# Kernel optimization log

Hardware: AMD Instinct MI355X
Metric: run time of the kernel (lower is better)

## Reference

```python
import jax, jax.numpy as jnp
import numpy as np

N_NODES = 100000


def sage_conv(x, src, dst, w_self, w_nei, b):
    # mean aggregation over incoming edges (src -> dst)
    agg = jax.ops.segment_sum(x[src], dst, num_segments=N_NODES)          # [N, d]
    deg = jax.ops.segment_sum(jnp.ones((src.shape[0], 1), x.dtype), dst,
                              num_segments=N_NODES)                        # [N, 1]
    mean = agg / jnp.maximum(deg, 1.0)
    return x @ w_self + mean @ w_nei + b


def setup_inputs() -> dict:
    key = jax.random.key(0)
    ks = jax.random.split(key, 12)
    d_in, d_hid, d_out = 64, 64, 64
    E = 1600000
    s = lambda d: 1.0 / np.sqrt(d)
    return {
        "x": jax.random.normal(ks[0], (N_NODES, d_in), jnp.float32),
        "edge_index": jax.random.randint(ks[1], (2, E), 0, N_NODES, jnp.int64),
        "w_self1": jax.random.normal(ks[2], (d_in, d_hid), jnp.float32) * s(d_in),
        "w_nei1": jax.random.normal(ks[3], (d_in, d_hid), jnp.float32) * s(d_in),
        "b1": jnp.zeros((d_hid,), jnp.float32),
        "w_self2": jax.random.normal(ks[4], (d_hid, d_hid), jnp.float32) * s(d_hid),
        "w_nei2": jax.random.normal(ks[5], (d_hid, d_hid), jnp.float32) * s(d_hid),
        "b2": jnp.zeros((d_hid,), jnp.float32),
        "w_self3": jax.random.normal(ks[6], (d_hid, d_out), jnp.float32) * s(d_hid),
        "w_nei3": jax.random.normal(ks[7], (d_hid, d_out), jnp.float32) * s(d_hid),
        "b3": jnp.zeros((d_out,), jnp.float32),
    }


def reference(x, edge_index, w_self1, w_nei1, b1, w_self2, w_nei2, b2,
              w_self3, w_nei3, b3):
    src, dst = edge_index[0], edge_index[1]
    h = jax.nn.relu(sage_conv(x, src, dst, w_self1, w_nei1, b1))
    h = jax.nn.relu(sage_conv(h, src, dst, w_self2, w_nei2, b2))
    h = sage_conv(h, src, dst, w_self3, w_nei3, b3)
    return h
```

## Files before the change

kernel.cpp:

```cpp
#include <hip/hip_runtime.h>
#include <hip/hip_bf16.h>

#define PB   512
#define BN   64
#define CAP  1344

typedef short bf16x8 __attribute__((ext_vector_type(8)));
typedef float f32x4  __attribute__((ext_vector_type(4)));

__device__ __forceinline__ unsigned short f2bf(float f) {
    unsigned u = __float_as_uint(f);
    u += 0x7FFFu + ((u >> 16) & 1u);
    return (unsigned short)(u >> 16);
}

__global__ __launch_bounds__(256) void build_and_prep(
        const int* __restrict__ src, const int* __restrict__ dst,
        int* __restrict__ gcount, int* __restrict__ pairs, int E, int NB,
        const float* __restrict__ x,
        unsigned short* __restrict__ xlo, unsigned short* __restrict__ xhi, int n8,
        const float* __restrict__ Ws1, const float* __restrict__ Wn1,
        const float* __restrict__ Ws2, const float* __restrict__ Wn2,
        const float* __restrict__ Ws3, const float* __restrict__ Wn3,
        unsigned short* __restrict__ bw) {
    const int tid = threadIdx.x;
    if (blockIdx.x < PB) {
        __shared__ int h[1664];
        for (int i = tid; i < NB; i += 256) h[i] = 0;
        __syncthreads();
        const int per = (E + PB - 1) / PB;
        const int s = blockIdx.x * per;
        const int e = min(E, s + per);
        for (int i = s + tid; i < e; i += 256) atomicAdd(&h[dst[i] >> 6], 1);
        __syncthreads();
        for (int b = tid; b < NB; b += 256) {
            const int c = h[b];
            h[b] = (c > 0) ? atomicAdd(&gcount[b], c) : 0;
        }
        __syncthreads();
        for (int i = s + tid; i < e; i += 256) {
            const int d = dst[i];
            const int b = d >> 6;
            const int slot = atomicAdd(&h[b], 1);
            if (slot < CAP)
                pairs[(size_t)b * CAP + slot] = src[i] | ((d & 63) << 20);
        }
    } else if (blockIdx.x < PB + 96) {
        const int i = (blockIdx.x - PB) * 256 + tid;
        const int w = i >> 13;
        const int r = i & 8191;
        const float* Ws = (w == 0) ? Ws1 : (w == 1) ? Ws2 : Ws3;
        const float* Wn = (w == 0) ? Wn1 : (w == 1) ? Wn2 : Wn3;
        const int j = r & 7;
        const int L = (r >> 3) & 63;
        const int t = (r >> 9) & 3;
        const int s = r >> 11;
        const int k = s * 32 + ((L >> 4) << 3) + j;
        const int n = t * 16 + (L & 15);
        const float v = (k < 64) ? Ws[k * 64 + n] : Wn[(k - 64) * 64 + n];
        bw[i] = f2bf(v);
    } else {
        const int g = (blockIdx.x - PB - 96) * 256 + tid;
        if (g >= n8) return;
        const float4 v0 = *(const float4*)(x + (size_t)g * 8);
        const float4 v1 = *(const float4*)(x + (size_t)g * 8 + 4);
        uint4 o;
        o.x = (unsigned)f2bf(v0.x) | ((unsigned)f2bf(v0.y) << 16);
        o.y = (unsigned)f2bf(v0.z) | ((unsigned)f2bf(v0.w) << 16);
        o.z = (unsigned)f2bf(v1.x) | ((unsigned)f2bf(v1.y) << 16);
        o.w = (unsigned)f2bf(v1.z) | ((unsigned)f2bf(v1.w) << 16);
        const int n = g >> 3;
        const int c = (g & 7) * 8;
        unsigned short* dstp = (c < 32) ? (xlo + (size_t)n * 32 + c)
                                        : (xhi + (size_t)n * 32 + (c - 32));
        *(uint4*)dstp = o;
    }
}

__global__ __launch_bounds__(256) void csr_finalize(const int* __restrict__ pairs,
                                                    const int* __restrict__ gcount,
                                                    int2* __restrict__ rowrange,
                                                    int* __restrict__ col, int N) {
    __shared__ int sp[CAP];
    __shared__ int h[64];
    __shared__ int tmp[64];
    __shared__ int cur[64];
    const int tid = threadIdx.x;
    const int b = blockIdx.x;
    const size_t base = (size_t)b * CAP;
    const int cnt = min(gcount[b], (int)CAP);

    for (int i = tid; i < cnt; i += 256) sp[i] = pairs[base + i];
    if (tid < 64) h[tid] = 0;
    __syncthreads();
    for (int i = tid; i < cnt; i += 256)
        atomicAdd(&h[(sp[i] >> 20) & 63], 1);
    __syncthreads();
    if (tid < 64) tmp[tid] = h[tid];
    __syncthreads();
    for (int off = 1; off < 64; off <<= 1) {
        int t = (tid >= off && tid < 64) ? tmp[tid - off] : 0;
        __syncthreads();
        if (tid < 64) tmp[tid] += t;
        __syncthreads();
    }
    if (tid < 64) {
        const int v = h[tid];
        const int excl = tmp[tid] - v;
        const int node = (b << 6) + tid;
        if (node < N) rowrange[node] = make_int2((int)base + excl, (int)base + excl + v);
        cur[tid] = excl;
    }
    __syncthreads();
    for (int i = tid; i < cnt; i += 256) {
        const int p = sp[i];
        const int slot = atomicAdd(&cur[(p >> 20) & 63], 1);
        col[base + slot] = p & 0xFFFFF;
    }
}

#define ACC8U(A, V)                                                   \
    A[0] += __uint_as_float((V).x << 16);                             \
    A[1] += __uint_as_float((V).x & 0xFFFF0000u);                     \
    A[2] += __uint_as_float((V).y << 16);                             \
    A[3] += __uint_as_float((V).y & 0xFFFF0000u);                     \
    A[4] += __uint_as_float((V).z << 16);                             \
    A[5] += __uint_as_float((V).z & 0xFFFF0000u);                     \
    A[6] += __uint_as_float((V).w << 16);                             \
    A[7] += __uint_as_float((V).w & 0xFFFF0000u);

__global__ __launch_bounds__(128) void sage_fused_kernel(
        const unsigned short* __restrict__ xlo, const unsigned short* __restrict__ xhi,
        const int* __restrict__ col, const int2* __restrict__ rowrange,
        const unsigned short* __restrict__ bswp, const float* __restrict__ bias,
        unsigned short* __restrict__ outlo,
        unsigned short* __restrict__ outhi,
        float* __restrict__ outf,
        int N, int do_relu) {
    __shared__ __align__(16) unsigned short smean[32][72];

    const int tid = threadIdx.x;
    const int node0 = blockIdx.x * 32;
    const int lane = tid & 63;

    {
        const int nl = tid >> 2;
        const int node = node0 + nl;
        const int o = (tid & 3) * 8;
        int beg = 0, end = 0;
        float rd = 0.f;
        if (node < N) {
            const int2 rr = rowrange[node];
            beg = rr.x;
            end = rr.y;
            rd = 1.0f / fmaxf((float)(end - beg), 1.0f);
        }
        const unsigned short* bases[2] = {xlo, xhi};
#pragma unroll
        for (int p = 0; p < 2; ++p) {
            const unsigned short* B = bases[p];
            float acc0[8] = {0.f}, acc1[8] = {0.f};
            int i = beg;
            for (; i + 8 <= end; i += 8) {
                int s[8];
#pragma unroll
                for (int k = 0; k < 8; ++k) s[k] = col[i + k];
                uint4 v[8];
#pragma unroll
                for (int k = 0; k < 8; ++k)
                    v[k] = *(const uint4*)(B + (size_t)s[k] * 32 + o);
#pragma unroll
                for (int k = 0; k < 8; k += 2) {
                    ACC8U(acc0, v[k]) ACC8U(acc1, v[k + 1])
                }
            }
            if (i + 4 <= end) {
                int s[4];
#pragma unroll
                for (int k = 0; k < 4; ++k) s[k] = col[i + k];
                uint4 v[4];
#pragma unroll
                for (int k = 0; k < 4; ++k)
                    v[k] = *(const uint4*)(B + (size_t)s[k] * 32 + o);
                ACC8U(acc0, v[0]) ACC8U(acc1, v[1])
                ACC8U(acc0, v[2]) ACC8U(acc1, v[3])
                i += 4;
            }
            for (; i < end; ++i) {
                const uint4 v = *(const uint4*)(B + (size_t)col[i] * 32 + o);
                ACC8U(acc0, v)
            }
            float m[8];
#pragma unroll
            for (int k = 0; k < 8; ++k) m[k] = (acc0[k] + acc1[k]) * rd;
            uint4 ov;
            ov.x = (unsigned)f2bf(m[0]) | ((unsigned)f2bf(m[1]) << 16);
            ov.y = (unsigned)f2bf(m[2]) | ((unsigned)f2bf(m[3]) << 16);
            ov.z = (unsigned)f2bf(m[4]) | ((unsigned)f2bf(m[5]) << 16);
            ov.w = (unsigned)f2bf(m[6]) | ((unsigned)f2bf(m[7]) << 16);
            *(uint4*)(&smean[nl][p * 32 + o]) = ov;
        }
    }
    __syncthreads();

    const int wave = tid >> 6;
    const int m    = lane & 15;
    const int quad = lane >> 4;
    const int nw0  = node0 + wave * 16;

    int arow = nw0 + m;
    if (arow >= N) arow = N - 1;
    const unsigned short* xrl = xlo + (size_t)arow * 32 + quad * 8;
    const unsigned short* xrh = xhi + (size_t)arow * 32 + quad * 8;

    f32x4 acc[4];
#pragma unroll
    for (int t = 0; t < 4; ++t) {
        const float b = bias[t * 16 + m];
        acc[t] = (f32x4){b, b, b, b};
    }

#pragma unroll
    for (int s = 0; s < 4; ++s) {
        bf16x8 a;
        if (s == 0)      a = *(const bf16x8*)(xrl);
        else if (s == 1) a = *(const bf16x8*)(xrh);
        else             a = *(const bf16x8*)(&smean[wave * 16 + m][(s - 2) * 32 + quad * 8]);
#pragma unroll
        for (int t = 0; t < 4; ++t) {
            const bf16x8 bf = *(const bf16x8*)(bswp + (((s * 4 + t) * 64 + lane) << 3));
            acc[t] = __builtin_amdgcn_mfma_f32_16x16x32_bf16(a, bf, acc[t], 0, 0, 0);
        }
    }

#pragma unroll
    for (int t = 0; t < 4; ++t) {
        const int colg = t * 16 + m;
#pragma unroll
        for (int r = 0; r < 4; ++r) {
            const int node = nw0 + quad * 4 + r;
            if (node < N) {
                float v = acc[t][r];
                if (do_relu) v = fmaxf(v, 0.f);
                if (outf) outf[(size_t)node * 64 + colg] = v;
                if (outlo) {
                    if (colg < 32) outlo[(size_t)node * 32 + colg]        = f2bf(v);
                    else           outhi[(size_t)node * 32 + (colg - 32)] = f2bf(v);
                }
            }
        }
    }
}

extern "C" void kernel_launch(void* const* d_in, const int* in_sizes, int n_in,
                              void* d_out, int out_size, void* d_ws, size_t ws_size,
                              hipStream_t stream) {
    const float* x   = (const float*)d_in[0];
    const int*   ei  = (const int*)d_in[1];
    const float* ws1 = (const float*)d_in[2];
    const float* wn1 = (const float*)d_in[3];
    const float* b1  = (const float*)d_in[4];
    const float* ws2 = (const float*)d_in[5];
    const float* wn2 = (const float*)d_in[6];
    const float* b2  = (const float*)d_in[7];
    const float* ws3 = (const float*)d_in[8];
    const float* wn3 = (const float*)d_in[9];
    const float* b3  = (const float*)d_in[10];

    const int N = in_sizes[0] / 64;
    const int E = in_sizes[1] / 2;
    const int* src = ei;
    const int* dst = ei + E;
    const int NB = (N + BN - 1) / BN;

    float* out = (float*)d_out;

    auto align256 = [](size_t v) { return (v + 255) / 256 * 256; };
    char* p = (char*)d_ws;
    int*  gcount   = (int*)p;  p += align256((size_t)NB * 4);
    int*  pairs    = (int*)p;  p += align256((size_t)NB * CAP * 4);
    int*  col      = (int*)p;  p += align256((size_t)NB * CAP * 4);
    int2* rowrange = (int2*)p; p += align256((size_t)N * 8);
    unsigned short* xlo  = (unsigned short*)p; p += align256((size_t)N * 32 * 2);
    unsigned short* xhi  = (unsigned short*)p; p += align256((size_t)N * 32 * 2);
    unsigned short* xlo2 = (unsigned short*)p; p += align256((size_t)N * 32 * 2);
    unsigned short* xhi2 = (unsigned short*)p; p += align256((size_t)N * 32 * 2);
    unsigned short* bw   = (unsigned short*)p; p += align256(3 * 8192 * 2);

    const int n8 = N * 64 / 8;
    const int merged_blocks = PB + 96 + (n8 + 255) / 256;
    const int fused_blocks = (N + 31) / 32;

    hipMemsetAsync(gcount, 0, (size_t)NB * 4, stream);
    build_and_prep<<<merged_blocks, 256, 0, stream>>>(src, dst, gcount, pairs, E, NB,
                                                      x, xlo, xhi, n8,
                                                      ws1, wn1, ws2, wn2, ws3, wn3, bw);
    csr_finalize<<<NB, 256, 0, stream>>>(pairs, gcount, rowrange, col, N);

    sage_fused_kernel<<<fused_blocks, 128, 0, stream>>>(xlo,  xhi,  col, rowrange, bw,         b1, xlo2, xhi2, nullptr, N, 1);
    sage_fused_kernel<<<fused_blocks, 128, 0, stream>>>(xlo2, xhi2, col, rowrange, bw + 8192,  b2, xlo,  xhi,  nullptr, N, 1);
    sage_fused_kernel<<<fused_blocks, 128, 0, stream>>>(xlo,  xhi,  col, rowrange, bw + 16384, b3, nullptr, nullptr, out, N, 0);
}
```

Baseline: 286.4 us.

## Gather neighbor features as per-row int8 with scales instead of bf16

Result: faster. 263.9 us (-7.8%).

```diff
diff --git a/kernel.cpp b/kernel.cpp
--- a/kernel.cpp
+++ b/kernel.cpp
@@ -14,11 +14,18 @@
     return (unsigned short)(u >> 16);
 }
 
+#define ACCB(A, i0, w, s)                                                \
+    A[i0 + 0] = fmaf((float)(((int)((w) << 24)) >> 24), s, A[i0 + 0]);   \
+    A[i0 + 1] = fmaf((float)(((int)((w) << 16)) >> 24), s, A[i0 + 1]);   \
+    A[i0 + 2] = fmaf((float)(((int)((w) <<  8)) >> 24), s, A[i0 + 2]);   \
+    A[i0 + 3] = fmaf((float)(((int)(w)) >> 24),         s, A[i0 + 3]);
+#define ACCQ4(A, V, s) { ACCB(A, 0, (V).x, s) ACCB(A, 4, (V).y, s) ACCB(A, 8, (V).z, s) ACCB(A, 12, (V).w, s) }
+
 __global__ __launch_bounds__(256) void build_and_prep(
         const int* __restrict__ src, const int* __restrict__ dst,
         int* __restrict__ gcount, int* __restrict__ pairs, int E, int NB,
-        const float* __restrict__ x,
-        unsigned short* __restrict__ xlo, unsigned short* __restrict__ xhi, int n8,
+        const float* __restrict__ x, unsigned short* __restrict__ xb,
+        unsigned char* __restrict__ xq, float* __restrict__ xs, int n8,
         const float* __restrict__ Ws1, const float* __restrict__ Wn1,
         const float* __restrict__ Ws2, const float* __restrict__ Wn2,
         const float* __restrict__ Ws3, const float* __restrict__ Wn3,
@@ -69,11 +76,22 @@
         o.y = (unsigned)f2bf(v0.z) | ((unsigned)f2bf(v0.w) << 16);
         o.z = (unsigned)f2bf(v1.x) | ((unsigned)f2bf(v1.y) << 16);
         o.w = (unsigned)f2bf(v1.z) | ((unsigned)f2bf(v1.w) << 16);
-        const int n = g >> 3;
-        const int c = (g & 7) * 8;
-        unsigned short* dstp = (c < 32) ? (xlo + (size_t)n * 32 + c)
-                                        : (xhi + (size_t)n * 32 + (c - 32));
-        *(uint4*)dstp = o;
+        *(uint4*)(xb + (size_t)g * 8) = o;
+        const float v8[8] = {v0.x, v0.y, v0.z, v0.w, v1.x, v1.y, v1.z, v1.w};
+        float mx = 0.f;
+#pragma unroll
+        for (int k = 0; k < 8; ++k) mx = fmaxf(mx, fabsf(v8[k]));
+#pragma unroll
+        for (int k = 1; k < 8; k <<= 1) mx = fmaxf(mx, __shfl_xor(mx, k, 64));
+        const float rs = (mx > 0.f) ? 127.f / mx : 0.f;
+        const int row = g >> 3;
+        if ((g & 7) == 0) xs[row] = (mx > 0.f) ? mx / 127.f : 0.f;
+        unsigned q0 = 0, q1 = 0;
+#pragma unroll
+        for (int k = 0; k < 4; ++k) q0 |= ((unsigned)__float2int_rn(v8[k] * rs) & 255u) << (8 * k);
+#pragma unroll
+        for (int k = 0; k < 4; ++k) q1 |= ((unsigned)__float2int_rn(v8[4 + k] * rs) & 255u) << (8 * k);
+        *(uint2*)(xq + (size_t)row * 64 + (g & 7) * 8) = make_uint2(q0, q1);
     }
 }
 
@@ -119,22 +137,15 @@
     }
 }
 
-#define ACC8U(A, V)                                                   \
-    A[0] += __uint_as_float((V).x << 16);                             \
-    A[1] += __uint_as_float((V).x & 0xFFFF0000u);                     \
-    A[2] += __uint_as_float((V).y << 16);                             \
-    A[3] += __uint_as_float((V).y & 0xFFFF0000u);                     \
-    A[4] += __uint_as_float((V).z << 16);                             \
-    A[5] += __uint_as_float((V).z & 0xFFFF0000u);                     \
-    A[6] += __uint_as_float((V).w << 16);                             \
-    A[7] += __uint_as_float((V).w & 0xFFFF0000u);
-
 __global__ __launch_bounds__(128) void sage_fused_kernel(
-        const unsigned short* __restrict__ xlo, const unsigned short* __restrict__ xhi,
+        const unsigned short* __restrict__ xin,
+        const unsigned char* __restrict__ xq,
+        const float* __restrict__ xs,
         const int* __restrict__ col, const int2* __restrict__ rowrange,
         const unsigned short* __restrict__ bswp, const float* __restrict__ bias,
-        unsigned short* __restrict__ outlo,
-        unsigned short* __restrict__ outhi,
+        unsigned short* __restrict__ outb,
+        unsigned char* __restrict__ outq,
+        float* __restrict__ outs,
         float* __restrict__ outf,
         int N, int do_relu) {
     __shared__ __align__(16) unsigned short smean[32][72];
@@ -146,60 +157,61 @@
     {
         const int nl = tid >> 2;
         const int node = node0 + nl;
-        const int o = (tid & 3) * 8;
-        int beg = 0, end = 0;
+        const int c16 = (tid & 3) * 16;
+        float acc[16];
+#pragma unroll
+        for (int k = 0; k < 16; ++k) acc[k] = 0.f;
         float rd = 0.f;
         if (node < N) {
             const int2 rr = rowrange[node];
-            beg = rr.x;
-            end = rr.y;
-            rd = 1.0f / fmaxf((float)(end - beg), 1.0f);
-        }
-        const unsigned short* bases[2] = {xlo, xhi};
-#pragma unroll
-        for (int p = 0; p < 2; ++p) {
-            const unsigned short* B = bases[p];
-            float acc0[8] = {0.f}, acc1[8] = {0.f};
+            const int beg = rr.x, end = rr.y;
             int i = beg;
             for (; i + 8 <= end; i += 8) {
                 int s[8];
 #pragma unroll
                 for (int k = 0; k < 8; ++k) s[k] = col[i + k];
-                uint4 v[8];
-#pragma unroll
-                for (int k = 0; k < 8; ++k)
-                    v[k] = *(const uint4*)(B + (size_t)s[k] * 32 + o);
-#pragma unroll
-                for (int k = 0; k < 8; k += 2) {
-                    ACC8U(acc0, v[k]) ACC8U(acc1, v[k + 1])
+                uint4 v[8]; float sc[8];
+#pragma unroll
+                for (int k = 0; k < 8; ++k) {
+                    v[k]  = *(const uint4*)(xq + (size_t)s[k] * 64 + c16);
+                    sc[k] = xs[s[k]];
                 }
+#pragma unroll
+                for (int k = 0; k < 8; ++k) { ACCQ4(acc, v[k], sc[k]) }
             }
             if (i + 4 <= end) {
                 int s[4];
 #pragma unroll
                 for (int k = 0; k < 4; ++k) s[k] = col[i + k];
-                uint4 v[4];
-#pragma unroll
-                for (int k = 0; k < 4; ++k)
-                    v[k] = *(const uint4*)(B + (size_t)s[k] * 32 + o);
-                ACC8U(acc0, v[0]) ACC8U(acc1, v[1])
-                ACC8U(acc0, v[2]) ACC8U(acc1, v[3])
+                uint4 v[4]; float sc[4];
+#pragma unroll
+                for (int k = 0; k < 4; ++k) {
+                    v[k]  = *(const uint4*)(xq + (size_t)s[k] * 64 + c16);
+                    sc[k] = xs[s[k]];
+                }
+#pragma unroll
+                for (int k = 0; k < 4; ++k) { ACCQ4(acc, v[k], sc[k]) }
                 i += 4;
             }
             for (; i < end; ++i) {
-                const uint4 v = *(const uint4*)(B + (size_t)col[i] * 32 + o);
-                ACC8U(acc0, v)
-            }
-            float m[8];
-#pragma unroll
-            for (int k = 0; k < 8; ++k) m[k] = (acc0[k] + acc1[k]) * rd;
-            uint4 ov;
-            ov.x = (unsigned)f2bf(m[0]) | ((unsigned)f2bf(m[1]) << 16);
-            ov.y = (unsigned)f2bf(m[2]) | ((unsigned)f2bf(m[3]) << 16);
-            ov.z = (unsigned)f2bf(m[4]) | ((unsigned)f2bf(m[5]) << 16);
-            ov.w = (unsigned)f2bf(m[6]) | ((unsigned)f2bf(m[7]) << 16);
-            *(uint4*)(&smean[nl][p * 32 + o]) = ov;
-        }
+                const int s = col[i];
+                const uint4 v = *(const uint4*)(xq + (size_t)s * 64 + c16);
+                const float sc = xs[s];
+                ACCQ4(acc, v, sc)
+            }
+            rd = 1.0f / fmaxf((float)(end - beg), 1.0f);
+        }
+        uint4 o0, o1;
+        o0.x = (unsigned)f2bf(acc[0] * rd)  | ((unsigned)f2bf(acc[1] * rd) << 16);
+        o0.y = (unsigned)f2bf(acc[2] * rd)  | ((unsigned)f2bf(acc[3] * rd) << 16);
+        o0.z = (unsigned)f2bf(acc[4] * rd)  | ((unsigned)f2bf(acc[5] * rd) << 16);
+        o0.w = (unsigned)f2bf(acc[6] * rd)  | ((unsigned)f2bf(acc[7] * rd) << 16);
+        o1.x = (unsigned)f2bf(acc[8] * rd)  | ((unsigned)f2bf(acc[9] * rd) << 16);
+        o1.y = (unsigned)f2bf(acc[10] * rd) | ((unsigned)f2bf(acc[11] * rd) << 16);
+        o1.z = (unsigned)f2bf(acc[12] * rd) | ((unsigned)f2bf(acc[13] * rd) << 16);
+        o1.w = (unsigned)f2bf(acc[14] * rd) | ((unsigned)f2bf(acc[15] * rd) << 16);
+        *(uint4*)(&smean[nl][c16])     = o0;
+        *(uint4*)(&smean[nl][c16 + 8]) = o1;
     }
     __syncthreads();
 
@@ -210,8 +222,7 @@
 
     int arow = nw0 + m;
     if (arow >= N) arow = N - 1;
-    const unsigned short* xrl = xlo + (size_t)arow * 32 + quad * 8;
-    const unsigned short* xrh = xhi + (size_t)arow * 32 + quad * 8;
+    const unsigned short* xr = xin + (size_t)arow * 64 + quad * 8;
 
     f32x4 acc[4];
 #pragma unroll
@@ -223,9 +234,8 @@
 #pragma unroll
     for (int s = 0; s < 4; ++s) {
         bf16x8 a;
-        if (s == 0)      a = *(const bf16x8*)(xrl);
-        else if (s == 1) a = *(const bf16x8*)(xrh);
-        else             a = *(const bf16x8*)(&smean[wave * 16 + m][(s - 2) * 32 + quad * 8]);
+        if (s < 2) a = *(const bf16x8*)(xr + s * 32);
+        else       a = *(const bf16x8*)(&smean[wave * 16 + m][(s - 2) * 32 + quad * 8]);
 #pragma unroll
         for (int t = 0; t < 4; ++t) {
             const bf16x8 bf = *(const bf16x8*)(bswp + (((s * 4 + t) * 64 + lane) << 3));
@@ -235,17 +245,41 @@
 
 #pragma unroll
     for (int t = 0; t < 4; ++t) {
+#pragma unroll
+        for (int r = 0; r < 4; ++r) {
+            float v = acc[t][r];
+            if (do_relu) v = fmaxf(v, 0.f);
+            acc[t][r] = v;
+        }
+    }
+#pragma unroll
+    for (int t = 0; t < 4; ++t) {
         const int colg = t * 16 + m;
 #pragma unroll
         for (int r = 0; r < 4; ++r) {
             const int node = nw0 + quad * 4 + r;
             if (node < N) {
-                float v = acc[t][r];
-                if (do_relu) v = fmaxf(v, 0.f);
-                if (outf) outf[(size_t)node * 64 + colg] = v;
-                if (outlo) {
-                    if (colg < 32) outlo[(size_t)node * 32 + colg]        = f2bf(v);
-                    else           outhi[(size_t)node * 32 + (colg - 32)] = f2bf(v);
+                if (outf) outf[(size_t)node * 64 + colg] = acc[t][r];
+                if (outb) outb[(size_t)node * 64 + colg] = f2bf(acc[t][r]);
+            }
+        }
+    }
+
+    if (outq) {
+#pragma unroll
+        for (int r = 0; r < 4; ++r) {
+            float mx = fmaxf(fmaxf(fabsf(acc[0][r]), fabsf(acc[1][r])),
+                             fmaxf(fabsf(acc[2][r]), fabsf(acc[3][r])));
+#pragma unroll
+            for (int k = 1; k < 16; k <<= 1) mx = fmaxf(mx, __shfl_xor(mx, k, 64));
+            const int node = nw0 + quad * 4 + r;
+            const float rs = (mx > 0.f) ? 127.f / mx : 0.f;
+            if (node < N) {
+                if (m == 0) outs[node] = (mx > 0.f) ? mx / 127.f : 0.f;
+#pragma unroll
+                for (int t = 0; t < 4; ++t) {
+                    const int q = __float2int_rn(acc[t][r] * rs);
+                    outq[(size_t)node * 64 + t * 16 + m] = (unsigned char)q;
                 }
             }
         }
@@ -281,11 +315,13 @@
     int*  pairs    = (int*)p;  p += align256((size_t)NB * CAP * 4);
     int*  col      = (int*)p;  p += align256((size_t)NB * CAP * 4);
     int2* rowrange = (int2*)p; p += align256((size_t)N * 8);
-    unsigned short* xlo  = (unsigned short*)p; p += align256((size_t)N * 32 * 2);
-    unsigned short* xhi  = (unsigned short*)p; p += align256((size_t)N * 32 * 2);
-    unsigned short* xlo2 = (unsigned short*)p; p += align256((size_t)N * 32 * 2);
-    unsigned short* xhi2 = (unsigned short*)p; p += align256((size_t)N * 32 * 2);
-    unsigned short* bw   = (unsigned short*)p; p += align256(3 * 8192 * 2);
+    unsigned short* xb  = (unsigned short*)p; p += align256((size_t)N * 64 * 2);
+    unsigned short* xb2 = (unsigned short*)p; p += align256((size_t)N * 64 * 2);
+    unsigned char*  xq  = (unsigned char*)p;  p += align256((size_t)N * 64);
+    unsigned char*  xq2 = (unsigned char*)p;  p += align256((size_t)N * 64);
+    float* xs  = (float*)p; p += align256((size_t)N * 4);
+    float* xs2 = (float*)p; p += align256((size_t)N * 4);
+    unsigned short* bw  = (unsigned short*)p; p += align256(3 * 8192 * 2);
 
     const int n8 = N * 64 / 8;
     const int merged_blocks = PB + 96 + (n8 + 255) / 256;
@@ -293,11 +329,11 @@
 
     hipMemsetAsync(gcount, 0, (size_t)NB * 4, stream);
     build_and_prep<<<merged_blocks, 256, 0, stream>>>(src, dst, gcount, pairs, E, NB,
-                                                      x, xlo, xhi, n8,
+                                                      x, xb, xq, xs, n8,
                                                       ws1, wn1, ws2, wn2, ws3, wn3, bw);
     csr_finalize<<<NB, 256, 0, stream>>>(pairs, gcount, rowrange, col, N);
 
-    sage_fused_kernel<<<fused_blocks, 128, 0, stream>>>(xlo,  xhi,  col, rowrange, bw,         b1, xlo2, xhi2, nullptr, N, 1);
-    sage_fused_kernel<<<fused_blocks, 128, 0, stream>>>(xlo2, xhi2, col, rowrange, bw + 8192,  b2, xlo,  xhi,  nullptr, N, 1);
-    sage_fused_kernel<<<fused_blocks, 128, 0, stream>>>(xlo,  xhi,  col, rowrange, bw + 16384, b3, nullptr, nullptr, out, N, 0);
-}
+    sage_fused_kernel<<<fused_blocks, 128, 0, stream>>>(xb,  xq,  xs,  col, rowrange, bw,         b1, xb2, xq2, xs2, nullptr, N, 1);
+    sage_fused_kernel<<<fused_blocks, 128, 0, stream>>>(xb2, xq2, xs2, col, rowrange, bw + 8192,  b2, xb,  xq,  xs,  nullptr, N, 1);
+    sage_fused_kernel<<<fused_blocks, 128, 0, stream>>>(xb,  xq,  xs,  col, rowrange, bw + 16384, b3, nullptr, nullptr, nullptr, out, N, 0);
+}
```

## Store bf16 features as contiguous 128B rows and use 256-thread blocks

Applied to the files above, without the earlier changes.

Result: faster. 277.2 us (-3.2%).

```diff
diff --git a/kernel.cpp b/kernel.cpp
--- a/kernel.cpp
+++ b/kernel.cpp
@@ -14,11 +14,20 @@
     return (unsigned short)(u >> 16);
 }
 
+#define ACC8U(A, V)                                                   \
+    A[0] += __uint_as_float((V).x << 16);                             \
+    A[1] += __uint_as_float((V).x & 0xFFFF0000u);                     \
+    A[2] += __uint_as_float((V).y << 16);                             \
+    A[3] += __uint_as_float((V).y & 0xFFFF0000u);                     \
+    A[4] += __uint_as_float((V).z << 16);                             \
+    A[5] += __uint_as_float((V).z & 0xFFFF0000u);                     \
+    A[6] += __uint_as_float((V).w << 16);                             \
+    A[7] += __uint_as_float((V).w & 0xFFFF0000u);
+
 __global__ __launch_bounds__(256) void build_and_prep(
         const int* __restrict__ src, const int* __restrict__ dst,
         int* __restrict__ gcount, int* __restrict__ pairs, int E, int NB,
-        const float* __restrict__ x,
-        unsigned short* __restrict__ xlo, unsigned short* __restrict__ xhi, int n8,
+        const float* __restrict__ x, unsigned short* __restrict__ xb, int n8,
         const float* __restrict__ Ws1, const float* __restrict__ Wn1,
         const float* __restrict__ Ws2, const float* __restrict__ Wn2,
         const float* __restrict__ Ws3, const float* __restrict__ Wn3,
@@ -69,11 +78,7 @@
         o.y = (unsigned)f2bf(v0.z) | ((unsigned)f2bf(v0.w) << 16);
         o.z = (unsigned)f2bf(v1.x) | ((unsigned)f2bf(v1.y) << 16);
         o.w = (unsigned)f2bf(v1.z) | ((unsigned)f2bf(v1.w) << 16);
-        const int n = g >> 3;
-        const int c = (g & 7) * 8;
-        unsigned short* dstp = (c < 32) ? (xlo + (size_t)n * 32 + c)
-                                        : (xhi + (size_t)n * 32 + (c - 32));
-        *(uint4*)dstp = o;
+        *(uint4*)(xb + (size_t)g * 8) = o;
     }
 }
 
@@ -119,22 +124,11 @@
     }
 }
 
-#define ACC8U(A, V)                                                   \
-    A[0] += __uint_as_float((V).x << 16);                             \
-    A[1] += __uint_as_float((V).x & 0xFFFF0000u);                     \
-    A[2] += __uint_as_float((V).y << 16);                             \
-    A[3] += __uint_as_float((V).y & 0xFFFF0000u);                     \
-    A[4] += __uint_as_float((V).z << 16);                             \
-    A[5] += __uint_as_float((V).z & 0xFFFF0000u);                     \
-    A[6] += __uint_as_float((V).w << 16);                             \
-    A[7] += __uint_as_float((V).w & 0xFFFF0000u);
-
-__global__ __launch_bounds__(128) void sage_fused_kernel(
-        const unsigned short* __restrict__ xlo, const unsigned short* __restrict__ xhi,
-        const int* __restrict__ col, const int2* __restrict__ rowrange,
+__global__ __launch_bounds__(256, 2) void sage_fused_kernel(
+        const unsigned short* __restrict__ xin, const int* __restrict__ col,
+        const int2* __restrict__ rowrange,
         const unsigned short* __restrict__ bswp, const float* __restrict__ bias,
-        unsigned short* __restrict__ outlo,
-        unsigned short* __restrict__ outhi,
+        unsigned short* __restrict__ outb,
         float* __restrict__ outf,
         int N, int do_relu) {
     __shared__ __align__(16) unsigned short smean[32][72];
@@ -144,35 +138,37 @@
     const int lane = tid & 63;
 
     {
-        const int nl = tid >> 2;
+        const int nl = tid >> 3;
         const int node = node0 + nl;
-        const int o = (tid & 3) * 8;
-        int beg = 0, end = 0;
+        const int o = (tid & 7) * 8;
+        float acc[8] = {0.f, 0.f, 0.f, 0.f, 0.f, 0.f, 0.f, 0.f};
         float rd = 0.f;
         if (node < N) {
             const int2 rr = rowrange[node];
-            beg = rr.x;
-            end = rr.y;
-            rd = 1.0f / fmaxf((float)(end - beg), 1.0f);
-        }
-        const unsigned short* bases[2] = {xlo, xhi};
-#pragma unroll
-        for (int p = 0; p < 2; ++p) {
-            const unsigned short* B = bases[p];
-            float acc0[8] = {0.f}, acc1[8] = {0.f};
+            const int beg = rr.x, end = rr.y;
             int i = beg;
-            for (; i + 8 <= end; i += 8) {
+            for (; i + 16 <= end; i += 16) {
+                int s[16];
+#pragma unroll
+                for (int k = 0; k < 16; ++k) s[k] = col[i + k];
+                uint4 v[16];
+#pragma unroll
+                for (int k = 0; k < 16; ++k)
+                    v[k] = *(const uint4*)(xin + (size_t)s[k] * 64 + o);
+#pragma unroll
+                for (int k = 0; k < 16; ++k) { ACC8U(acc, v[k]) }
+            }
+            if (i + 8 <= end) {
                 int s[8];
 #pragma unroll
                 for (int k = 0; k < 8; ++k) s[k] = col[i + k];
                 uint4 v[8];
 #pragma unroll
                 for (int k = 0; k < 8; ++k)
-                    v[k] = *(const uint4*)(B + (size_t)s[k] * 32 + o);
-#pragma unroll
-                for (int k = 0; k < 8; k += 2) {
-                    ACC8U(acc0, v[k]) ACC8U(acc1, v[k + 1])
-                }
+                    v[k] = *(const uint4*)(xin + (size_t)s[k] * 64 + o);
+#pragma unroll
+                for (int k = 0; k < 8; ++k) { ACC8U(acc, v[k]) }
+                i += 8;
             }
             if (i + 4 <= end) {
                 int s[4];
@@ -181,72 +177,68 @@
                 uint4 v[4];
 #pragma unroll
                 for (int k = 0; k < 4; ++k)
-                    v[k] = *(const uint4*)(B + (size_t)s[k] * 32 + o);
-                ACC8U(acc0, v[0]) ACC8U(acc1, v[1])
-                ACC8U(acc0, v[2]) ACC8U(acc1, v[3])
+                    v[k] = *(const uint4*)(xin + (size_t)s[k] * 64 + o);
+#pragma unroll
+                for (int k = 0; k < 4; ++k) { ACC8U(acc, v[k]) }
                 i += 4;
             }
             for (; i < end; ++i) {
-                const uint4 v = *(const uint4*)(B + (size_t)col[i] * 32 + o);
-                ACC8U(acc0, v)
-            }
-            float m[8];
-#pragma unroll
-            for (int k = 0; k < 8; ++k) m[k] = (acc0[k] + acc1[k]) * rd;
-            uint4 ov;
-            ov.x = (unsigned)f2bf(m[0]) | ((unsigned)f2bf(m[1]) << 16);
-            ov.y = (unsigned)f2bf(m[2]) | ((unsigned)f2bf(m[3]) << 16);
-            ov.z = (unsigned)f2bf(m[4]) | ((unsigned)f2bf(m[5]) << 16);
-            ov.w = (unsigned)f2bf(m[6]) | ((unsigned)f2bf(m[7]) << 16);
-            *(uint4*)(&smean[nl][p * 32 + o]) = ov;
-        }
+                const uint4 v = *(const uint4*)(xin + (size_t)col[i] * 64 + o);
+                ACC8U(acc, v)
+            }
+            rd = 1.0f / fmaxf((float)(end - beg), 1.0f);
+        }
+        uint4 ov;
+        ov.x = (unsigned)f2bf(acc[0] * rd) | ((unsigned)f2bf(acc[1] * rd) << 16);
+        ov.y = (unsigned)f2bf(acc[2] * rd) | ((unsigned)f2bf(acc[3] * rd) << 16);
+        ov.z = (unsigned)f2bf(acc[4] * rd) | ((unsigned)f2bf(acc[5] * rd) << 16);
+        ov.w = (unsigned)f2bf(acc[6] * rd) | ((unsigned)f2bf(acc[7] * rd) << 16);
+        *(uint4*)(&smean[nl][o]) = ov;
     }
     __syncthreads();
 
     const int wave = tid >> 6;
     const int m    = lane & 15;
     const int quad = lane >> 4;
-    const int nw0  = node0 + wave * 16;
+    const int nh   = wave & 1;
+    const int th   = wave >> 1;
+    const int nw0  = node0 + nh * 16;
 
     int arow = nw0 + m;
     if (arow >= N) arow = N - 1;
-    const unsigned short* xrl = xlo + (size_t)arow * 32 + quad * 8;
-    const unsigned short* xrh = xhi + (size_t)arow * 32 + quad * 8;
-
-    f32x4 acc[4];
-#pragma unroll
-    for (int t = 0; t < 4; ++t) {
-        const float b = bias[t * 16 + m];
-        acc[t] = (f32x4){b, b, b, b};
+    const unsigned short* xr = xin + (size_t)arow * 64 + quad * 8;
+
+    f32x4 acc[2];
+#pragma unroll
+    for (int j = 0; j < 2; ++j) {
+        const float b = bias[(th * 2 + j) * 16 + m];
+        acc[j] = (f32x4){b, b, b, b};
     }
 
 #pragma unroll
     for (int s = 0; s < 4; ++s) {
         bf16x8 a;
-        if (s == 0)      a = *(const bf16x8*)(xrl);
-        else if (s == 1) a = *(const bf16x8*)(xrh);
-        else             a = *(const bf16x8*)(&smean[wave * 16 + m][(s - 2) * 32 + quad * 8]);
-#pragma unroll
-        for (int t = 0; t < 4; ++t) {
+        if (s < 2) a = *(const bf16x8*)(xr + s * 32);
+        else       a = *(const bf16x8*)(&smean[nh * 16 + m][(s - 2) * 32 + quad * 8]);
+#pragma unroll
+        for (int j = 0; j < 2; ++j) {
+            const int t = th * 2 + j;
             const bf16x8 bf = *(const bf16x8*)(bswp + (((s * 4 + t) * 64 + lane) << 3));
-            acc[t] = __builtin_amdgcn_mfma_f32_16x16x32_bf16(a, bf, acc[t], 0, 0, 0);
-        }
-    }
-
-#pragma unroll
-    for (int t = 0; t < 4; ++t) {
-        const int colg = t * 16 + m;
+            acc[j] = __builtin_amdgcn_mfma_f32_16x16x32_bf16(a, bf, acc[j], 0, 0, 0);
+        }
+    }
+
+#pragma unroll
+    for (int j = 0; j < 2; ++j) {
+        const int colg = (th * 2 + j) * 16 + m;
 #pragma unroll
         for (int r = 0; r < 4; ++r) {
             const int node = nw0 + quad * 4 + r;
             if (node < N) {
-                float v = acc[t][r];
+                float v = acc[j][r];
                 if (do_relu) v = fmaxf(v, 0.f);
                 if (outf) outf[(size_t)node * 64 + colg] = v;
-                if (outlo) {
-                    if (colg < 32) outlo[(size_t)node * 32 + colg]        = f2bf(v);
-                    else           outhi[(size_t)node * 32 + (colg - 32)] = f2bf(v);
-                }
+                if (outb) outb[(size_t)node * 64 + colg] = f2bf(v);
             }
         }
     }
@@ -281,11 +273,9 @@
     int*  pairs    = (int*)p;  p += align256((size_t)NB * CAP * 4);
     int*  col      = (int*)p;  p += align256((size_t)NB * CAP * 4);
     int2* rowrange = (int2*)p; p += align256((size_t)N * 8);
-    unsigned short* xlo  = (unsigned short*)p; p += align256((size_t)N * 32 * 2);
-    unsigned short* xhi  = (unsigned short*)p; p += align256((size_t)N * 32 * 2);
-    unsigned short* xlo2 = (unsigned short*)p; p += align256((size_t)N * 32 * 2);
-    unsigned short* xhi2 = (unsigned short*)p; p += align256((size_t)N * 32 * 2);
-    unsigned short* bw   = (unsigned short*)p; p += align256(3 * 8192 * 2);
+    unsigned short* xb  = (unsigned short*)p; p += align256((size_t)N * 64 * 2);
+    unsigned short* xb2 = (unsigned short*)p; p += align256((size_t)N * 64 * 2);
+    unsigned short* bw  = (unsigned short*)p; p += align256(3 * 8192 * 2);
 
     const int n8 = N * 64 / 8;
     const int merged_blocks = PB + 96 + (n8 + 255) / 256;
@@ -293,11 +283,11 @@
 
     hipMemsetAsync(gcount, 0, (size_t)NB * 4, stream);
     build_and_prep<<<merged_blocks, 256, 0, stream>>>(src, dst, gcount, pairs, E, NB,
-                                                      x, xlo, xhi, n8,
+                                                      x, xb, n8,
                                                       ws1, wn1, ws2, wn2, ws3, wn3, bw);
     csr_finalize<<<NB, 256, 0, stream>>>(pairs, gcount, rowrange, col, N);
 
-    sage_fused_kernel<<<fused_blocks, 128, 0, stream>>>(xlo,  xhi,  col, rowrange, bw,         b1, xlo2, xhi2, nullptr, N, 1);
-    sage_fused_kernel<<<fused_blocks, 128, 0, stream>>>(xlo2, xhi2, col, rowrange, bw + 8192,  b2, xlo,  xhi,  nullptr, N, 1);
-    sage_fused_kernel<<<fused_blocks, 128, 0, stream>>>(xlo,  xhi,  col, rowrange, bw + 16384, b3, nullptr, nullptr, out, N, 0);
-}
+    sage_fused_kernel<<<fused_blocks, 256, 0, stream>>>(xb,  col, rowrange, bw,         b1, xb2,     nullptr, N, 1);
+    sage_fused_kernel<<<fused_blocks, 256, 0, stream>>>(xb2, col, rowrange, bw + 8192,  b2, xb,      nullptr, N, 1);
+    sage_fused_kernel<<<fused_blocks, 256, 0, stream>>>(xb,  col, rowrange, bw + 16384, b3, nullptr, out,     N, 0);
+}
```
